# Kernel optimization log

Hardware: AMD Instinct MI355X
Metric: run time of the kernel (lower is better)

## Reference

```python
import jax, jax.numpy as jnp
import numpy as np

B, T, NMELS = 512, 180, 40
HID, NLAYER, PROJ = 768, 3, 256


def _lstm_layer(x, w_ih, w_hh, b):
    """PyTorch-convention LSTM layer. x: [B, T, D] -> h_seq: [B, T, H].
    Gate order i, f, g, o. b = b_ih + b_hh."""
    Bn = x.shape[0]
    H = w_hh.shape[1]
    # Input contribution for all timesteps at once: [T, B, 4H]
    xg = jnp.einsum('btd,gd->tbg', x, w_ih) + b

    def step(carry, xg_t):
        h, c = carry
        g = xg_t + h @ w_hh.T  # [B, 4H]
        i, f, gg, o = jnp.split(g, 4, axis=-1)
        i = jax.nn.sigmoid(i)
        f = jax.nn.sigmoid(f)
        gg = jnp.tanh(gg)
        o = jax.nn.sigmoid(o)
        c = f * c + i * gg
        h = o * jnp.tanh(c)
        return (h, c), h

    h0 = jnp.zeros((Bn, H), x.dtype)
    c0 = jnp.zeros((Bn, H), x.dtype)
    (_, _), hs = jax.lax.scan(step, (h0, c0), xg)  # hs: [T, B, H]
    return jnp.transpose(hs, (1, 0, 2))


def setup_inputs() -> dict:
    key = jax.random.key(0)
    ks = jax.random.split(key, 16)
    G = 4 * HID

    def xavier(k, shape):
        fan_out, fan_in = shape
        std = np.sqrt(2.0 / (fan_in + fan_out)).astype(np.float32)
        return jax.random.normal(k, shape, jnp.float32) * std

    inp = {
        'x': jax.random.normal(ks[0], (B, T, NMELS), jnp.float32),
        'w_ih0': xavier(ks[1], (G, NMELS)),
        'w_hh0': xavier(ks[2], (G, HID)),
        'b_ih0': jnp.zeros((G,), jnp.float32),
        'b_hh0': jnp.zeros((G,), jnp.float32),
        'w_ih1': xavier(ks[3], (G, HID)),
        'w_hh1': xavier(ks[4], (G, HID)),
        'b_ih1': jnp.zeros((G,), jnp.float32),
        'b_hh1': jnp.zeros((G,), jnp.float32),
        'w_ih2': xavier(ks[5], (G, HID)),
        'w_hh2': xavier(ks[6], (G, HID)),
        'b_ih2': jnp.zeros((G,), jnp.float32),
        'b_hh2': jnp.zeros((G,), jnp.float32),
        'proj_w': xavier(ks[7], (PROJ, HID)),
        'proj_b': jnp.zeros((PROJ,), jnp.float32),
    }
    return inp


def reference(x, w_ih0, w_hh0, b_ih0, b_hh0,
              w_ih1, w_hh1, b_ih1, b_hh1,
              w_ih2, w_hh2, b_ih2, b_hh2,
              proj_w, proj_b):
    h = _lstm_layer(x, w_ih0, w_hh0, b_ih0 + b_hh0)
    h = _lstm_layer(h, w_ih1, w_hh1, b_ih1 + b_hh1)
    h = _lstm_layer(h, w_ih2, w_hh2, b_ih2 + b_hh2)
    last = h[:, -1]                       # [B, HID] last timestep
    e = last @ proj_w.T + proj_b          # [B, PROJ]
    e = e / jnp.linalg.norm(e, axis=1, keepdims=True)
    return e
```

## Files before the change

kernel.cpp:

```cpp
#include <hip/hip_runtime.h>
#include <cstdint>
#include <cstddef>

using u16 = unsigned short;
using u32 = unsigned int;

typedef __attribute__((ext_vector_type(8)))  __bf16 bf16x8;
typedef __attribute__((ext_vector_type(16))) float  f32x16;

constexpr int kB   = 512;
constexpr int kT   = 180;
constexpr int kH   = 768;
constexpr int NBLK = 192;

constexpr int L0N  = 16 * 192 * 832;
constexpr int L12N = 16 * 192 * 1536;

constexpr int RING_SLOT_E = 24 * 512 * 32;
constexpr size_t RING_SZ  = (size_t)2 * RING_SLOT_E * 2;

constexpr size_t OFF_R0  = 256;
constexpr size_t OFF_R1  = OFF_R0 + RING_SZ;
constexpr size_t OFF_R2  = OFF_R1 + RING_SZ;
constexpr size_t OFF_PB  = OFF_R2 + RING_SZ;
constexpr size_t OFF_XT  = OFF_PB + (size_t)3 * 3072 * 4;
constexpr size_t OFF_W0  = OFF_XT + (size_t)kT * kB * 64 * 2;
constexpr size_t OFF_W1  = OFF_W0 + (size_t)L0N * 2;
constexpr size_t OFF_W2  = OFF_W1 + (size_t)L12N * 2;
constexpr size_t WS_NEED = OFF_W2 + (size_t)L12N * 2;

#define CLB __asm__ volatile("" ::: "memory")

__device__ __forceinline__ float bf2f(u16 u) {
  union { u32 i; float f; } v; v.i = ((u32)u) << 16; return v.f;
}
__device__ __forceinline__ u16 f2bf(float f) {
  union { float f; u32 i; } v; v.f = f;
  u32 r = v.i + 0x7fffu + ((v.i >> 16) & 1u);
  return (u16)(r >> 16);
}

typedef __attribute__((address_space(1))) const u32 as1_u32;
typedef __attribute__((address_space(3))) u32 as3_u32;
__device__ __forceinline__ void gload_lds16(const u16* g, u16* l) {
  __builtin_amdgcn_global_load_lds((as1_u32*)g, (as3_u32*)l, 16, 0, 0);
}

__global__ void k_zero(uint4* p, int n) {
  uint4 z = make_uint4(0u, 0u, 0u, 0u);
  for (int i = blockIdx.x * 256 + threadIdx.x; i < n; i += gridDim.x * 256) p[i] = z;
}

__global__ void k_pack_w(const float* __restrict__ wih0, const float* __restrict__ whh0,
                         const float* __restrict__ wih1, const float* __restrict__ whh1,
                         const float* __restrict__ wih2, const float* __restrict__ whh2,
                         u16* __restrict__ W0, u16* __restrict__ W1, u16* __restrict__ W2) {
  int idx = blockIdx.x * 256 + threadIdx.x;
  if (idx < L0N) {
    int col = idx / 832, k = idx - col * 832;
    int ntile = col / 192, p = col - ntile * 192;
    int g = p / 48, hc = p - g * 48;
    int gcol = g * 768 + ntile * 48 + hc;
    float v = (k < 40) ? wih0[gcol * 40 + k]
                       : ((k < 64) ? 0.f : whh0[(size_t)gcol * 768 + (k - 64)]);
    W0[idx] = f2bf(v);
  } else if (idx < L0N + L12N) {
    int li = idx - L0N;
    int col = li / 1536, k = li - col * 1536;
    int ntile = col / 192, p = col - ntile * 192;
    int g = p / 48, hc = p - g * 48;
    int gcol = g * 768 + ntile * 48 + hc;
    float v = (k < 768) ? wih1[(size_t)gcol * 768 + k] : whh1[(size_t)gcol * 768 + (k - 768)];
    W1[li] = f2bf(v);
  } else {
    int li = idx - (L0N + L12N);
    if (li < L12N) {
      int col = li / 1536, k = li - col * 1536;
      int ntile = col / 192, p = col - ntile * 192;
      int g = p / 48, hc = p - g * 48;
      int gcol = g * 768 + ntile * 48 + hc;
      float v = (k < 768) ? wih2[(size_t)gcol * 768 + k] : whh2[(size_t)gcol * 768 + (k - 768)];
      W2[li] = f2bf(v);
    }
  }
}

__global__ void k_pack_b(const float* __restrict__ bi0, const float* __restrict__ bh0,
                         const float* __restrict__ bi1, const float* __restrict__ bh1,
                         const float* __restrict__ bi2, const float* __restrict__ bh2,
                         float* __restrict__ pbo) {
  int idx = blockIdx.x * 256 + threadIdx.x;
  int l = idx / 3072, r = idx - l * 3072;
  int ntile = r / 192, p = r - ntile * 192;
  int g = p / 48, hc = p - g * 48;
  int gcol = g * 768 + ntile * 48 + hc;
  const float* bi = (l == 0) ? bi0 : ((l == 1) ? bi1 : bi2);
  const float* bh = (l == 0) ? bh0 : ((l == 1) ? bh1 : bh2);
  pbo[idx] = bi[gcol] + bh[gcol];
}

__global__ void k_xT(const float* __restrict__ x, u16* __restrict__ xT) {
  int idx = blockIdx.x * 256 + threadIdx.x;
  int t = idx / (512 * 64);
  int r = idx - t * 512 * 64;
  int b = r >> 6, j = r & 63;
  float v = (j < 40) ? x[((size_t)b * 180 + t) * 40 + j] : 0.f;
  xT[(size_t)t * 32768 + (size_t)(j >> 5) * 16384 + b * 32 + (j & 31)] = f2bf(v);
}

__global__ __launch_bounds__(256, 2) void k_lstm(
    const u16* __restrict__ xT,
    u16* __restrict__ ring0, u16* __restrict__ ring1, u16* __restrict__ ring2,
    const u16* __restrict__ W0, const u16* __restrict__ W1, const u16* __restrict__ W2,
    const float* __restrict__ pb, u32* __restrict__ bar) {
  __shared__ __align__(16) unsigned char smem[61440 + 768];
  u16*   scr = (u16*)smem;
  float* pbs = (float*)(smem + 61440);

  const int tid = threadIdx.x;
  const int bid = blockIdx.x;
  const int xcd = bid & 7, j0 = bid >> 3;
  const int g_    = (j0 >> 2) * 8 + xcd;
  const int mt    = j0 & 3;
  const int layer = g_ >> 4;
  const int ntile = g_ & 15;
  const int mrow0 = mt * 128;

  const u16* Wl     = (layer == 0) ? W0 : ((layer == 1) ? W1 : W2);
  const int  Kl     = (layer == 0) ? 832 : 1536;
  const int  KcIn   = (layer == 0) ? 2 : 24;
  const int  nch    = (layer == 0) ? 26 : 48;
  const u16* inseq  = (layer == 1) ? ring0 : ring1;
  u16*       ringS  = (layer == 0) ? ring0 : ((layer == 1) ? ring1 : ring2);
  const u16* bbase0 = Wl + (size_t)(ntile * 192) * Kl;

  for (int i = tid; i < 192; i += 256) pbs[i] = pb[layer * 3072 + ntile * 192 + i];

  const int wid = tid >> 6, lane = tid & 63;
  const int wm = wid & 1, wn = wid >> 1;
  const int l31 = lane & 31, lhi = lane >> 5;

  float c_reg[24];
#pragma unroll
  for (int i = 0; i < 24; i++) c_reg[i] = 0.f;

  for (int s = 0; s < kT + 2; ++s) {
    const int t = s - layer;
    if (t >= 0 && t < kT) {
      f32x16 acc[2][3];
#pragma unroll
      for (int mi = 0; mi < 2; mi++)
#pragma unroll
        for (int ni = 0; ni < 3; ni++)
#pragma unroll
          for (int r = 0; r < 16; r++) acc[mi][ni][r] = 0.f;

      const u16* inbase  = (layer == 0) ? (xT + (size_t)t * 32768)
                                        : (inseq + (size_t)(t & 1) * RING_SLOT_E);
      const u16* recbase = ringS + (size_t)((t - 1) & 1) * RING_SLOT_E;

      auto stage = [&](int c, int st) {
        u16* sbA = (u16*)(smem + st * 20480);
        u16* sbB = sbA + 4096;
        const u16* abase = (c < KcIn) ? (inbase + (size_t)c * 16384)
                                      : (recbase + (size_t)(c - KcIn) * 16384);
#pragma unroll
        for (int k = 0; k < 2; k++) {
          const int e = tid + k * 256;
          const int row = e >> 2, sp = e & 3;
          const int so = sp ^ ((row >> 1) & 3);
          gload_lds16(abase + (size_t)(mrow0 + row) * 32 + so * 8, sbA + (size_t)e * 8);
        }
        const u16* bb = bbase0 + c * 32;
#pragma unroll
        for (int k = 0; k < 3; k++) {
          const int e = tid + k * 256;
          const int col = e >> 2, sp = e & 3;
          const int so = sp ^ ((col >> 1) & 3);
          gload_lds16(bb + (size_t)col * Kl + so * 8, sbB + (size_t)e * 8);
        }
      };

      stage(0, 0);
      stage(1, 1);
      for (int c = 0; c < nch; ++c) {
        CLB;
        if (c == nch - 1) __builtin_amdgcn_s_waitcnt(0xF70);
        else              __builtin_amdgcn_s_waitcnt(0xF75);
        __builtin_amdgcn_s_barrier();
        CLB;
        if (c + 2 < nch) stage(c + 2, (c + 2) % 3);
        const u16* sA = (const u16*)(smem + (c % 3) * 20480);
        const u16* sB = sA + 4096;
        const int wsw = (l31 >> 1) & 3;
#pragma unroll
        for (int kk = 0; kk < 2; kk++) {
          const int sl = (((kk << 1) | lhi) ^ wsw) << 3;
          bf16x8 a0 = *(const bf16x8*)(sA + (wm * 64 +      l31) * 32 + sl);
          bf16x8 a1 = *(const bf16x8*)(sA + (wm * 64 + 32 + l31) * 32 + sl);
          const int c0 = wn * 96 + l31;
          bf16x8 b0 = *(const bf16x8*)(sB + (c0     ) * 32 + sl);
          bf16x8 b1 = *(const bf16x8*)(sB + (c0 + 32) * 32 + sl);
          bf16x8 b2 = *(const bf16x8*)(sB + (c0 + 64) * 32 + sl);
          acc[0][0] = __builtin_amdgcn_mfma_f32_32x32x16_bf16(a0, b0, acc[0][0], 0, 0, 0);
          acc[0][1] = __builtin_amdgcn_mfma_f32_32x32x16_bf16(a0, b1, acc[0][1], 0, 0, 0);
          acc[0][2] = __builtin_amdgcn_mfma_f32_32x32x16_bf16(a0, b2, acc[0][2], 0, 0, 0);
          acc[1][0] = __builtin_amdgcn_mfma_f32_32x32x16_bf16(a1, b0, acc[1][0], 0, 0, 0);
          acc[1][1] = __builtin_amdgcn_mfma_f32_32x32x16_bf16(a1, b1, acc[1][1], 0, 0, 0);
          acc[1][2] = __builtin_amdgcn_mfma_f32_32x32x16_bf16(a1, b2, acc[1][2], 0, 0, 0);
        }
      }
      __syncthreads();
#pragma unroll
      for (int mi = 0; mi < 2; mi++) {
#pragma unroll
        for (int ni = 0; ni < 3; ni++) {
          const int pcol = wn * 96 + ni * 32 + l31;
          const int gg = pcol / 48;
          const float bias = pbs[pcol];
#pragma unroll
          for (int r = 0; r < 16; r++) {
            const int rowl = wm * 64 + mi * 32 + (r & 3) + ((r >> 2) << 3) + (lhi << 2);
            float v = acc[mi][ni][r] + bias;
            v = (gg == 2) ? tanhf(v) : (1.f / (1.f + __expf(-v)));
            scr[rowl * 192 + pcol] = f2bf(v);
          }
        }
      }
      __syncthreads();
      u16* hout = ringS + (size_t)(t & 1) * RING_SLOT_E;
#pragma unroll
      for (int jj = 0; jj < 24; jj++) {
        const int idx = jj * 256 + tid;
        const int row = idx / 48;
        const int hc  = idx - row * 48;
        const float iv = bf2f(scr[row * 192       + hc]);
        const float fv = bf2f(scr[row * 192 +  48 + hc]);
        const float gv = bf2f(scr[row * 192 +  96 + hc]);
        const float ov = bf2f(scr[row * 192 + 144 + hc]);
        const float cn = fv * c_reg[jj] + iv * gv;
        c_reg[jj] = cn;
        const int colg = ntile * 48 + hc;
        hout[(size_t)(colg >> 5) * 16384 + (size_t)(mrow0 + row) * 32 + (colg & 31)]
            = f2bf(ov * tanhf(cn));
      }
    }
    __syncthreads();
    if (tid == 0) {
      __hip_atomic_fetch_add(bar, 1u, __ATOMIC_RELEASE, __HIP_MEMORY_SCOPE_AGENT);
      const u32 goal = (u32)(s + 1) * (u32)NBLK;
      u32 tries = 0;
      while (__hip_atomic_load(bar, __ATOMIC_RELAXED, __HIP_MEMORY_SCOPE_AGENT) < goal) {
        __builtin_amdgcn_s_sleep(8);
        if (++tries > 100000u) break;
      }
      __threadfence();
    }
    __syncthreads();
  }
}

__global__ __launch_bounds__(256) void k_proj(const u16* __restrict__ hlast,
                                              const float* __restrict__ pw,
                                              const float* __restrict__ pbv,
                                              float* __restrict__ out) {
  __shared__ float hs[8 * 768];
  __shared__ float wred[4 * 8];
  __shared__ float inv[8];
  const int tid = threadIdx.x;
  const int r0 = blockIdx.x * 8;
  for (int i = tid; i < 8 * 768; i += 256) {
    const int b = i / 768, col = i - b * 768;
    hs[i] = bf2f(hlast[(size_t)(col >> 5) * 16384 + (size_t)(r0 + b) * 32 + (col & 31)]);
  }
  __syncthreads();
  float acc[8];
#pragma unroll
  for (int r = 0; r < 8; r++) acc[r] = 0.f;
  const float* wrow = pw + (size_t)tid * 768;
  for (int k = 0; k < 768; k++) {
    float w = wrow[k];
#pragma unroll
    for (int r = 0; r < 8; r++) acc[r] += hs[r * 768 + k] * w;
  }
  const float bv = pbv[tid];
#pragma unroll
  for (int r = 0; r < 8; r++) acc[r] += bv;
  const int lane = tid & 63, w4 = tid >> 6;
#pragma unroll
  for (int r = 0; r < 8; r++) {
    float v = acc[r] * acc[r];
#pragma unroll
    for (int off = 32; off > 0; off >>= 1) v += __shfl_xor(v, off);
    if (lane == 0) wred[w4 * 8 + r] = v;
  }
  __syncthreads();
  if (tid < 8) {
    float sum = wred[tid] + wred[8 + tid] + wred[16 + tid] + wred[24 + tid];
    inv[tid] = 1.f / sqrtf(sum);
  }
  __syncthreads();
#pragma unroll
  for (int r = 0; r < 8; r++) out[(size_t)(r0 + r) * 256 + tid] = acc[r] * inv[r];
}

extern "C" void kernel_launch(void* const* d_in, const int* in_sizes, int n_in,
                              void* d_out, int out_size, void* d_ws, size_t ws_size,
                              hipStream_t stream) {
  const float* x    = (const float*)d_in[0];
  const float* wih0 = (const float*)d_in[1];
  const float* whh0 = (const float*)d_in[2];
  const float* bi0  = (const float*)d_in[3];
  const float* bh0  = (const float*)d_in[4];
  const float* wih1 = (const float*)d_in[5];
  const float* whh1 = (const float*)d_in[6];
  const float* bi1  = (const float*)d_in[7];
  const float* bh1  = (const float*)d_in[8];
  const float* wih2 = (const float*)d_in[9];
  const float* whh2 = (const float*)d_in[10];
  const float* bi2  = (const float*)d_in[11];
  const float* bh2  = (const float*)d_in[12];
  const float* pw   = (const float*)d_in[13];
  const float* pbv  = (const float*)d_in[14];

  if (ws_size < WS_NEED) return;

  char* ws  = (char*)d_ws;
  u32*  bar = (u32*)(ws + 0);
  u16*  r0  = (u16*)(ws + OFF_R0);
  u16*  r1  = (u16*)(ws + OFF_R1);
  u16*  r2  = (u16*)(ws + OFF_R2);
  float* pb = (float*)(ws + OFF_PB);
  u16*  xT  = (u16*)(ws + OFF_XT);
  u16*  W0  = (u16*)(ws + OFF_W0);
  u16*  W1  = (u16*)(ws + OFF_W1);
  u16*  W2  = (u16*)(ws + OFF_W2);

  hipLaunchKernelGGL(k_zero, dim3(512), dim3(256), 0, stream,
                     (uint4*)ws, (int)(OFF_PB / 16));
  hipLaunchKernelGGL(k_pack_w, dim3((L0N + 2 * L12N + 255) / 256), dim3(256), 0, stream,
                     wih0, whh0, wih1, whh1, wih2, whh2, W0, W1, W2);
  hipLaunchKernelGGL(k_pack_b, dim3(36), dim3(256), 0, stream,
                     bi0, bh0, bi1, bh1, bi2, bh2, pb);
  hipLaunchKernelGGL(k_xT, dim3(kT * kB * 64 / 256), dim3(256), 0, stream, x, xT);

  {
    const u16* xTc = xT; const float* pbc = pb;
    const u16 *W0c = W0, *W1c = W1, *W2c = W2;
    u16 *r0m = r0, *r1m = r1, *r2m = r2; u32* barm = bar;
    void* kargs[] = {(void*)&xTc, (void*)&r0m, (void*)&r1m, (void*)&r2m,
                     (void*)&W0c, (void*)&W1c, (void*)&W2c, (void*)&pbc, (void*)&barm};
    hipLaunchCooperativeKernel((void*)k_lstm, dim3(NBLK), dim3(256), kargs, 0, stream);
  }

  hipLaunchKernelGGL(k_proj, dim3(64), dim3(256), 0, stream,
                     r2 + (size_t)((kT - 1) & 1) * RING_SLOT_E, pw, pbv, (float*)d_out);
}
```

Before: 9.799 ms.

## Deepen LSTM LDS pipeline to six stages with dynamic shared memory

Adds a k_lstm_deep variant that uses about 120 KB of dynamic LDS for six prefetch stages instead of three. It keeps five chunks in flight, with vmcnt waits tuned to the remaining chunk count, and runs at one block per CU. Activation and recurrent loads now carry a cache-policy bit, and the __threadfence after the grid barrier spin is removed. The aim is to hide global-load latency in the per-timestep GEMM. The cost is lower occupancy and a reliance on the cache bits, rather than the fence, to make cross-block data visible.

```diff
diff --git a/kernel.cpp b/kernel.cpp
--- a/kernel.cpp
+++ b/kernel.cpp
@@ -29,6 +29,10 @@
 constexpr size_t OFF_W2  = OFF_W1 + (size_t)L12N * 2;
 constexpr size_t WS_NEED = OFF_W2 + (size_t)L12N * 2;
 
+constexpr int    NSTAGE   = 6;
+constexpr size_t STAGE_SZ = 20480;
+constexpr size_t DYN_LDS  = NSTAGE * STAGE_SZ + 768;
+
 #define CLB __asm__ volatile("" ::: "memory")
 
 __device__ __forceinline__ float bf2f(u16 u) {
@@ -44,6 +48,9 @@
 typedef __attribute__((address_space(3))) u32 as3_u32;
 __device__ __forceinline__ void gload_lds16(const u16* g, u16* l) {
   __builtin_amdgcn_global_load_lds((as1_u32*)g, (as3_u32*)l, 16, 0, 0);
+}
+__device__ __forceinline__ void gload_lds16_dc(const u16* g, u16* l) {
+  __builtin_amdgcn_global_load_lds((as1_u32*)g, (as3_u32*)l, 16, 0, 16);
 }
 
 __global__ void k_zero(uint4* p, int n) {
@@ -108,156 +115,171 @@
   xT[(size_t)t * 32768 + (size_t)(j >> 5) * 16384 + b * 32 + (j & 31)] = f2bf(v);
 }
 
+#define LSTM_BODY(SMEM_DECL, SMEM_PTR, NSTG, DEEP)                                     \
+  SMEM_DECL;                                                                           \
+  u16*   scr = (u16*)(SMEM_PTR);                                                       \
+  float* pbs = (float*)((SMEM_PTR) + (size_t)(NSTG) * STAGE_SZ);                       \
+  const int tid = threadIdx.x;                                                         \
+  const int bid = blockIdx.x;                                                          \
+  const int xcd = bid & 7, j0 = bid >> 3;                                              \
+  const int g_    = (j0 >> 2) * 8 + xcd;                                               \
+  const int mt    = j0 & 3;                                                            \
+  const int layer = g_ >> 4;                                                           \
+  const int ntile = g_ & 15;                                                           \
+  const int mrow0 = mt * 128;                                                          \
+  const u16* Wl     = (layer == 0) ? W0 : ((layer == 1) ? W1 : W2);                    \
+  const int  Kl     = (layer == 0) ? 832 : 1536;                                       \
+  const int  KcIn   = (layer == 0) ? 2 : 24;                                           \
+  const int  nch    = (layer == 0) ? 26 : 48;                                          \
+  const u16* inseq  = (layer == 1) ? ring0 : ring1;                                    \
+  u16*       ringS  = (layer == 0) ? ring0 : ((layer == 1) ? ring1 : ring2);           \
+  const u16* bbase0 = Wl + (size_t)(ntile * 192) * Kl;                                 \
+  for (int i = tid; i < 192; i += 256) pbs[i] = pb[layer * 3072 + ntile * 192 + i];    \
+  const int wid = tid >> 6, lane = tid & 63;                                           \
+  const int wm = wid & 1, wn = wid >> 1;                                               \
+  const int l31 = lane & 31, lhi = lane >> 5;                                          \
+  float c_reg[24];                                                                     \
+  _Pragma("unroll")                                                                    \
+  for (int i = 0; i < 24; i++) c_reg[i] = 0.f;                                         \
+  for (int s = 0; s < kT + 2; ++s) {                                                   \
+    const int t = s - layer;                                                           \
+    if (t >= 0 && t < kT) {                                                            \
+      f32x16 acc[2][3];                                                                \
+      _Pragma("unroll")                                                                \
+      for (int mi = 0; mi < 2; mi++)                                                   \
+        for (int ni = 0; ni < 3; ni++)                                                 \
+          for (int r = 0; r < 16; r++) acc[mi][ni][r] = 0.f;                           \
+      const u16* inbase  = (layer == 0) ? (xT + (size_t)t * 32768)                     \
+                                        : (inseq + (size_t)(t & 1) * RING_SLOT_E);     \
+      const u16* recbase = ringS + (size_t)((t - 1) & 1) * RING_SLOT_E;                \
+      auto stage = [&](int c, int st) {                                                \
+        u16* sbA = (u16*)((SMEM_PTR) + (size_t)st * STAGE_SZ);                         \
+        u16* sbB = sbA + 4096;                                                         \
+        const bool rsrc = (layer != 0) || (c >= KcIn);                                 \
+        const u16* abase = (c < KcIn) ? (inbase + (size_t)c * 16384)                   \
+                                      : (recbase + (size_t)(c - KcIn) * 16384);        \
+        _Pragma("unroll")                                                              \
+        for (int k = 0; k < 2; k++) {                                                  \
+          const int e = tid + k * 256;                                                 \
+          const int row = e >> 2, sp = e & 3;                                          \
+          const int so = sp ^ ((row >> 1) & 3);                                        \
+          const u16* ga = abase + (size_t)(mrow0 + row) * 32 + so * 8;                 \
+          u16*       la = sbA + (size_t)e * 8;                                         \
+          if (rsrc) gload_lds16_dc(ga, la);                                            \
+          else      gload_lds16(ga, la);                                               \
+        }                                                                              \
+        const u16* bb = bbase0 + c * 32;                                               \
+        _Pragma("unroll")                                                              \
+        for (int k = 0; k < 3; k++) {                                                  \
+          const int e = tid + k * 256;                                                 \
+          const int col = e >> 2, sp = e & 3;                                          \
+          const int so = sp ^ ((col >> 1) & 3);                                        \
+          gload_lds16(bb + (size_t)col * Kl + so * 8, sbB + (size_t)e * 8);            \
+        }                                                                              \
+      };                                                                               \
+      if (DEEP) { stage(0,0); stage(1,1); stage(2,2); stage(3,3); stage(4,4); }        \
+      else      { stage(0,0); stage(1,1); }                                            \
+      for (int c = 0; c < nch; ++c) {                                                  \
+        CLB;                                                                           \
+        const int rem = nch - 1 - c;                                                   \
+        if (DEEP) {                                                                    \
+          switch (rem > 4 ? 4 : rem) {                                                 \
+            case 0:  __builtin_amdgcn_s_waitcnt(0x0F70); break;         \
+            case 1:  __builtin_amdgcn_s_waitcnt(0x0F75); break;         \
+            case 2:  __builtin_amdgcn_s_waitcnt(0x0F7A); break;         \
+            case 3:  __builtin_amdgcn_s_waitcnt(0x0F7F); break;         \
+            default: __builtin_amdgcn_s_waitcnt(0x4F74); break;         \
+          }                                                                            \
+        } else {                                                                       \
+          if (rem == 0) __builtin_amdgcn_s_waitcnt(0x0F70);             \
+          else          __builtin_amdgcn_s_waitcnt(0x0F75);             \
+        }                                                                              \
+        __builtin_amdgcn_s_barrier();                                                  \
+        CLB;                                                                           \
+        const int pf = DEEP ? 5 : 2;                                                   \
+        if (c + pf < nch) stage(c + pf, (c + pf) % (NSTG));                            \
+        const u16* sA = (const u16*)((SMEM_PTR) + (size_t)(c % (NSTG)) * STAGE_SZ);    \
+        const u16* sB = sA + 4096;                                                     \
+        const int wsw = (l31 >> 1) & 3;                                                \
+        _Pragma("unroll")                                                              \
+        for (int kk = 0; kk < 2; kk++) {                                               \
+          const int sl = (((kk << 1) | lhi) ^ wsw) << 3;                               \
+          bf16x8 a0 = *(const bf16x8*)(sA + (wm * 64 +      l31) * 32 + sl);           \
+          bf16x8 a1 = *(const bf16x8*)(sA + (wm * 64 + 32 + l31) * 32 + sl);           \
+          const int c0 = wn * 96 + l31;                                                \
+          bf16x8 b0 = *(const bf16x8*)(sB + (c0     ) * 32 + sl);                      \
+          bf16x8 b1 = *(const bf16x8*)(sB + (c0 + 32) * 32 + sl);                      \
+          bf16x8 b2 = *(const bf16x8*)(sB + (c0 + 64) * 32 + sl);                      \
+          acc[0][0] = __builtin_amdgcn_mfma_f32_32x32x16_bf16(a0, b0, acc[0][0],0,0,0);\
+          acc[0][1] = __builtin_amdgcn_mfma_f32_32x32x16_bf16(a0, b1, acc[0][1],0,0,0);\
+          acc[0][2] = __builtin_amdgcn_mfma_f32_32x32x16_bf16(a0, b2, acc[0][2],0,0,0);\
+          acc[1][0] = __builtin_amdgcn_mfma_f32_32x32x16_bf16(a1, b0, acc[1][0],0,0,0);\
+          acc[1][1] = __builtin_amdgcn_mfma_f32_32x32x16_bf16(a1, b1, acc[1][1],0,0,0);\
+          acc[1][2] = __builtin_amdgcn_mfma_f32_32x32x16_bf16(a1, b2, acc[1][2],0,0,0);\
+        }                                                                              \
+      }                                                                                \
+      __syncthreads();                                                                 \
+      _Pragma("unroll")                                                                \
+      for (int mi = 0; mi < 2; mi++) {                                                 \
+        _Pragma("unroll")                                                              \
+        for (int ni = 0; ni < 3; ni++) {                                               \
+          const int pcol = wn * 96 + ni * 32 + l31;                                    \
+          const int gg = pcol / 48;                                                    \
+          const float bias = pbs[pcol];                                                \
+          _Pragma("unroll")                                                            \
+          for (int r = 0; r < 16; r++) {                                               \
+            const int rowl = wm * 64 + mi * 32 + (r & 3) + ((r >> 2) << 3) + (lhi << 2);\
+            float v = acc[mi][ni][r] + bias;                                           \
+            v = (gg == 2) ? tanhf(v) : (1.f / (1.f + __expf(-v)));                     \
+            scr[rowl * 192 + pcol] = f2bf(v);                                          \
+          }                                                                            \
+        }                                                                              \
+      }                                                                                \
+      __syncthreads();                                                                 \
+      u16* hout = ringS + (size_t)(t & 1) * RING_SLOT_E;                               \
+      _Pragma("unroll")                                                                \
+      for (int jj = 0; jj < 24; jj++) {                                                \
+        const int idx = jj * 256 + tid;                                                \
+        const int row = idx / 48;                                                      \
+        const int hc  = idx - row * 48;                                                \
+        const float iv = bf2f(scr[row * 192       + hc]);                              \
+        const float fv = bf2f(scr[row * 192 +  48 + hc]);                              \
+        const float gv = bf2f(scr[row * 192 +  96 + hc]);                              \
+        const float ov = bf2f(scr[row * 192 + 144 + hc]);                              \
+        const float cn = fv * c_reg[jj] + iv * gv;                                     \
+        c_reg[jj] = cn;                                                                \
+        const int colg = ntile * 48 + hc;                                              \
+        hout[(size_t)(colg >> 5) * 16384 + (size_t)(mrow0 + row) * 32 + (colg & 31)]   \
+            = f2bf(ov * tanhf(cn));                                                    \
+      }                                                                                \
+    }                                                                                  \
+    __syncthreads();                                                                   \
+    if (tid == 0) {                                                                    \
+      __hip_atomic_fetch_add(bar, 1u, __ATOMIC_RELEASE, __HIP_MEMORY_SCOPE_AGENT);     \
+      const u32 goal = (u32)(s + 1) * (u32)NBLK;                                       \
+      u32 tries = 0;                                                                   \
+      while (__hip_atomic_load(bar, __ATOMIC_RELAXED, __HIP_MEMORY_SCOPE_AGENT) < goal) {\
+        __builtin_amdgcn_s_sleep(8);                                                   \
+        if (++tries > 100000u) break;                                                  \
+      }                                                                                \
+    }                                                                                  \
+    __syncthreads();                                                                   \
+  }
+
+__global__ __launch_bounds__(256, 1) void k_lstm_deep(
+    const u16* __restrict__ xT,
+    u16* __restrict__ ring0, u16* __restrict__ ring1, u16* __restrict__ ring2,
+    const u16* __restrict__ W0, const u16* __restrict__ W1, const u16* __restrict__ W2,
+    const float* __restrict__ pb, u32* __restrict__ bar) {
+  LSTM_BODY(extern __shared__ __align__(16) unsigned char smem[], smem, NSTAGE, 1)
+}
+
 __global__ __launch_bounds__(256, 2) void k_lstm(
     const u16* __restrict__ xT,
     u16* __restrict__ ring0, u16* __restrict__ ring1, u16* __restrict__ ring2,
     const u16* __restrict__ W0, const u16* __restrict__ W1, const u16* __restrict__ W2,
     const float* __restrict__ pb, u32* __restrict__ bar) {
-  __shared__ __align__(16) unsigned char smem[61440 + 768];
-  u16*   scr = (u16*)smem;
-  float* pbs = (float*)(smem + 61440);
-
-  const int tid = threadIdx.x;
-  const int bid = blockIdx.x;
-  const int xcd = bid & 7, j0 = bid >> 3;
-  const int g_    = (j0 >> 2) * 8 + xcd;
-  const int mt    = j0 & 3;
-  const int layer = g_ >> 4;
-  const int ntile = g_ & 15;
-  const int mrow0 = mt * 128;
-
-  const u16* Wl     = (layer == 0) ? W0 : ((layer == 1) ? W1 : W2);
-  const int  Kl     = (layer == 0) ? 832 : 1536;
-  const int  KcIn   = (layer == 0) ? 2 : 24;
-  const int  nch    = (layer == 0) ? 26 : 48;
-  const u16* inseq  = (layer == 1) ? ring0 : ring1;
-  u16*       ringS  = (layer == 0) ? ring0 : ((layer == 1) ? ring1 : ring2);
-  const u16* bbase0 = Wl + (size_t)(ntile * 192) * Kl;
-
-  for (int i = tid; i < 192; i += 256) pbs[i] = pb[layer * 3072 + ntile * 192 + i];
-
-  const int wid = tid >> 6, lane = tid & 63;
-  const int wm = wid & 1, wn = wid >> 1;
-  const int l31 = lane & 31, lhi = lane >> 5;
-
-  float c_reg[24];
-#pragma unroll
-  for (int i = 0; i < 24; i++) c_reg[i] = 0.f;
-
-  for (int s = 0; s < kT + 2; ++s) {
-    const int t = s - layer;
-    if (t >= 0 && t < kT) {
-      f32x16 acc[2][3];
-#pragma unroll
-      for (int mi = 0; mi < 2; mi++)
-#pragma unroll
-        for (int ni = 0; ni < 3; ni++)
-#pragma unroll
-          for (int r = 0; r < 16; r++) acc[mi][ni][r] = 0.f;
-
-      const u16* inbase  = (layer == 0) ? (xT + (size_t)t * 32768)
-                                        : (inseq + (size_t)(t & 1) * RING_SLOT_E);
-      const u16* recbase = ringS + (size_t)((t - 1) & 1) * RING_SLOT_E;
-
-      auto stage = [&](int c, int st) {
-        u16* sbA = (u16*)(smem + st * 20480);
-        u16* sbB = sbA + 4096;
-        const u16* abase = (c < KcIn) ? (inbase + (size_t)c * 16384)
-                                      : (recbase + (size_t)(c - KcIn) * 16384);
-#pragma unroll
-        for (int k = 0; k < 2; k++) {
-          const int e = tid + k * 256;
-          const int row = e >> 2, sp = e & 3;
-          const int so = sp ^ ((row >> 1) & 3);
-          gload_lds16(abase + (size_t)(mrow0 + row) * 32 + so * 8, sbA + (size_t)e * 8);
-        }
-        const u16* bb = bbase0 + c * 32;
-#pragma unroll
-        for (int k = 0; k < 3; k++) {
-          const int e = tid + k * 256;
-          const int col = e >> 2, sp = e & 3;
-          const int so = sp ^ ((col >> 1) & 3);
-          gload_lds16(bb + (size_t)col * Kl + so * 8, sbB + (size_t)e * 8);
-        }
-      };
-
-      stage(0, 0);
-      stage(1, 1);
-      for (int c = 0; c < nch; ++c) {
-        CLB;
-        if (c == nch - 1) __builtin_amdgcn_s_waitcnt(0xF70);
-        else              __builtin_amdgcn_s_waitcnt(0xF75);
-        __builtin_amdgcn_s_barrier();
-        CLB;
-        if (c + 2 < nch) stage(c + 2, (c + 2) % 3);
-        const u16* sA = (const u16*)(smem + (c % 3) * 20480);
-        const u16* sB = sA + 4096;
-        const int wsw = (l31 >> 1) & 3;
-#pragma unroll
-        for (int kk = 0; kk < 2; kk++) {
-          const int sl = (((kk << 1) | lhi) ^ wsw) << 3;
-          bf16x8 a0 = *(const bf16x8*)(sA + (wm * 64 +      l31) * 32 + sl);
-          bf16x8 a1 = *(const bf16x8*)(sA + (wm * 64 + 32 + l31) * 32 + sl);
-          const int c0 = wn * 96 + l31;
-          bf16x8 b0 = *(const bf16x8*)(sB + (c0     ) * 32 + sl);
-          bf16x8 b1 = *(const bf16x8*)(sB + (c0 + 32) * 32 + sl);
-          bf16x8 b2 = *(const bf16x8*)(sB + (c0 + 64) * 32 + sl);
-          acc[0][0] = __builtin_amdgcn_mfma_f32_32x32x16_bf16(a0, b0, acc[0][0], 0, 0, 0);
-          acc[0][1] = __builtin_amdgcn_mfma_f32_32x32x16_bf16(a0, b1, acc[0][1], 0, 0, 0);
-          acc[0][2] = __builtin_amdgcn_mfma_f32_32x32x16_bf16(a0, b2, acc[0][2], 0, 0, 0);
-          acc[1][0] = __builtin_amdgcn_mfma_f32_32x32x16_bf16(a1, b0, acc[1][0], 0, 0, 0);
-          acc[1][1] = __builtin_amdgcn_mfma_f32_32x32x16_bf16(a1, b1, acc[1][1], 0, 0, 0);
-          acc[1][2] = __builtin_amdgcn_mfma_f32_32x32x16_bf16(a1, b2, acc[1][2], 0, 0, 0);
-        }
-      }
-      __syncthreads();
-#pragma unroll
-      for (int mi = 0; mi < 2; mi++) {
-#pragma unroll
-        for (int ni = 0; ni < 3; ni++) {
-          const int pcol = wn * 96 + ni * 32 + l31;
-          const int gg = pcol / 48;
-          const float bias = pbs[pcol];
-#pragma unroll
-          for (int r = 0; r < 16; r++) {
-            const int rowl = wm * 64 + mi * 32 + (r & 3) + ((r >> 2) << 3) + (lhi << 2);
-            float v = acc[mi][ni][r] + bias;
-            v = (gg == 2) ? tanhf(v) : (1.f / (1.f + __expf(-v)));
-            scr[rowl * 192 + pcol] = f2bf(v);
-          }
-        }
-      }
-      __syncthreads();
-      u16* hout = ringS + (size_t)(t & 1) * RING_SLOT_E;
-#pragma unroll
-      for (int jj = 0; jj < 24; jj++) {
-        const int idx = jj * 256 + tid;
-        const int row = idx / 48;
-        const int hc  = idx - row * 48;
-        const float iv = bf2f(scr[row * 192       + hc]);
-        const float fv = bf2f(scr[row * 192 +  48 + hc]);
-        const float gv = bf2f(scr[row * 192 +  96 + hc]);
-        const float ov = bf2f(scr[row * 192 + 144 + hc]);
-        const float cn = fv * c_reg[jj] + iv * gv;
-        c_reg[jj] = cn;
-        const int colg = ntile * 48 + hc;
-        hout[(size_t)(colg >> 5) * 16384 + (size_t)(mrow0 + row) * 32 + (colg & 31)]
-            = f2bf(ov * tanhf(cn));
-      }
-    }
-    __syncthreads();
-    if (tid == 0) {
-      __hip_atomic_fetch_add(bar, 1u, __ATOMIC_RELEASE, __HIP_MEMORY_SCOPE_AGENT);
-      const u32 goal = (u32)(s + 1) * (u32)NBLK;
-      u32 tries = 0;
-      while (__hip_atomic_load(bar, __ATOMIC_RELAXED, __HIP_MEMORY_SCOPE_AGENT) < goal) {
-        __builtin_amdgcn_s_sleep(8);
-        if (++tries > 100000u) break;
-      }
-      __threadfence();
-    }
-    __syncthreads();
-  }
+  LSTM_BODY(__shared__ __align__(16) unsigned char smem[61440 + 768], smem, 3, 0)
 }
 
 __global__ __launch_bounds__(256) void k_proj(const u16* __restrict__ hlast,
@@ -325,6 +347,17 @@
 
   if (ws_size < WS_NEED) return;
 
+  static int use_deep = -1;
+  if (use_deep < 0) {
+    hipError_t e1 = hipFuncSetAttribute((const void*)k_lstm_deep,
+                                        hipFuncAttributeMaxDynamicSharedMemorySize,
+                                        (int)DYN_LDS);
+    int nb = 0;
+    hipError_t e2 = hipOccupancyMaxActiveBlocksPerMultiprocessor(
+        &nb, k_lstm_deep, 256, (size_t)DYN_LDS);
+    use_deep = (e1 == hipSuccess && e2 == hipSuccess && nb >= 1) ? 1 : 0;
+  }
+
   char* ws  = (char*)d_ws;
   u32*  bar = (u32*)(ws + 0);
   u16*  r0  = (u16*)(ws + OFF_R0);
@@ -350,7 +383,12 @@
     u16 *r0m = r0, *r1m = r1, *r2m = r2; u32* barm = bar;
     void* kargs[] = {(void*)&xTc, (void*)&r0m, (void*)&r1m, (void*)&r2m,
                      (void*)&W0c, (void*)&W1c, (void*)&W2c, (void*)&pbc, (void*)&barm};
-    hipLaunchCooperativeKernel((void*)k_lstm, dim3(NBLK), dim3(256), kargs, 0, stream);
+    if (use_deep) {
+      hipLaunchCooperativeKernel((void*)k_lstm_deep, dim3(NBLK), dim3(256), kargs,
+                                 (unsigned int)DYN_LDS, stream);
+    } else {
+      hipLaunchCooperativeKernel((void*)k_lstm, dim3(NBLK), dim3(256), kargs, 0, stream);
+    }
   }
 
   hipLaunchKernelGGL(k_proj, dim3(64), dim3(256), 0, stream,
```

New measurement: 9.411 ms. -4.0%, faster.

## Replace global grid barrier with per-tile dataflow flags and split into 384 blocks

Applied to the files above, without the earlier changes.

Swaps the grid-wide barrier after every wavefront step for per-(layer, row-tile) counters: each block waits only for its input layer's tile, its own layer's previous step, and the next layer's progress, which lets the three layers pipeline loosely. A new 384-block variant halves the M tile to 64 rows with three blocks per CU, for more parallelism and less work per block on each step. The old 192-block kernel is kept as a fallback, chosen at runtime from an occupancy query. This adds more flag polling traffic and smaller MFMA tiles that reuse the B operand less.

```diff
diff --git a/kernel.cpp b/kernel.cpp
--- a/kernel.cpp
+++ b/kernel.cpp
@@ -11,7 +11,8 @@
 constexpr int kB   = 512;
 constexpr int kT   = 180;
 constexpr int kH   = 768;
-constexpr int NBLK = 192;
+constexpr int NBLK3 = 384;
+constexpr int NBLK2 = 192;
 
 constexpr int L0N  = 16 * 192 * 832;
 constexpr int L12N = 16 * 192 * 1536;
@@ -19,7 +20,7 @@
 constexpr int RING_SLOT_E = 24 * 512 * 32;
 constexpr size_t RING_SZ  = (size_t)2 * RING_SLOT_E * 2;
 
-constexpr size_t OFF_R0  = 256;
+constexpr size_t OFF_R0  = 16384;
 constexpr size_t OFF_R1  = OFF_R0 + RING_SZ;
 constexpr size_t OFF_R2  = OFF_R1 + RING_SZ;
 constexpr size_t OFF_PB  = OFF_R2 + RING_SZ;
@@ -108,11 +109,162 @@
   xT[(size_t)t * 32768 + (size_t)(j >> 5) * 16384 + b * 32 + (j & 31)] = f2bf(v);
 }
 
-__global__ __launch_bounds__(256, 2) void k_lstm(
+__global__ __launch_bounds__(256, 3) void k_lstm384(
     const u16* __restrict__ xT,
     u16* __restrict__ ring0, u16* __restrict__ ring1, u16* __restrict__ ring2,
     const u16* __restrict__ W0, const u16* __restrict__ W1, const u16* __restrict__ W2,
-    const float* __restrict__ pb, u32* __restrict__ bar) {
+    const float* __restrict__ pb, u32* __restrict__ flg) {
+  __shared__ __align__(16) unsigned char smem[49152];
+  u16* scr = (u16*)smem;
+
+  const int tid = threadIdx.x;
+  const int bid = blockIdx.x;
+  const int xcd = bid & 7, j0 = bid >> 3;
+  const int g_    = (j0 >> 3) * 8 + xcd;
+  const int mt    = j0 & 7;
+  const int layer = g_ >> 4;
+  const int ntile = g_ & 15;
+  const int mrow0 = mt * 64;
+
+  const u16* Wl     = (layer == 0) ? W0 : ((layer == 1) ? W1 : W2);
+  const int  Kl     = (layer == 0) ? 832 : 1536;
+  const int  KcIn   = (layer == 0) ? 2 : 24;
+  const int  nch    = (layer == 0) ? 26 : 48;
+  const u16* inseq  = (layer == 1) ? ring0 : ring1;
+  u16*       ringS  = (layer == 0) ? ring0 : ((layer == 1) ? ring1 : ring2);
+  const u16* bbase0 = Wl + (size_t)(ntile * 192) * Kl;
+
+  u32* Fself = flg + (size_t)(((layer << 3) | mt) * 64);
+  u32* Fin   = flg + (size_t)((((layer - 1) << 3) | mt) * 64);
+  u32* Fnxt  = flg + (size_t)((((layer + 1) << 3) | mt) * 64);
+
+  const int wid = tid >> 6, lane = tid & 63;
+  const int wm = wid & 1, wn = wid >> 1;
+  const int l31 = lane & 31, lhi = lane >> 5;
+
+  float bias_r[3];
+#pragma unroll
+  for (int ni = 0; ni < 3; ni++)
+    bias_r[ni] = pb[layer * 3072 + ntile * 192 + wn * 96 + ni * 32 + l31];
+
+  float c_reg[12];
+#pragma unroll
+  for (int i = 0; i < 12; i++) c_reg[i] = 0.f;
+
+  for (int t = 0; t < kT; ++t) {
+    if (tid == 0) {
+      auto spinf = [&](u32* f, u32 goal) {
+        u32 tries = 0;
+        while (__hip_atomic_load(f, __ATOMIC_RELAXED, __HIP_MEMORY_SCOPE_AGENT) < goal) {
+          __builtin_amdgcn_s_sleep(4);
+          if (++tries > 400000u) break;
+        }
+      };
+      if (layer >= 1)           spinf(Fin,   16u * (u32)(t + 1));
+      if (t >= 1)               spinf(Fself, 16u * (u32)t);
+      if (layer <= 1 && t >= 2) spinf(Fnxt,  16u * (u32)(t - 1));
+      __threadfence();
+    }
+    __syncthreads();
+
+    f32x16 acc[3];
+#pragma unroll
+    for (int ni = 0; ni < 3; ni++)
+#pragma unroll
+      for (int r = 0; r < 16; r++) acc[ni][r] = 0.f;
+
+    const u16* inbase  = (layer == 0) ? (xT + (size_t)t * 32768)
+                                      : (inseq + (size_t)(t & 1) * RING_SLOT_E);
+    const u16* recbase = ringS + (size_t)((t - 1) & 1) * RING_SLOT_E;
+
+    auto stage = [&](int c, int st) {
+      u16* sbA = (u16*)(smem + (size_t)st * 16384);
+      u16* sbB = sbA + 2048;
+      const u16* abase = (c < KcIn) ? (inbase + (size_t)c * 16384)
+                                    : (recbase + (size_t)(c - KcIn) * 16384);
+      {
+        const int e = tid;
+        const int row = e >> 2, sp = e & 3;
+        const int so = sp ^ ((row >> 1) & 3);
+        gload_lds16(abase + (size_t)(mrow0 + row) * 32 + so * 8, sbA + (size_t)e * 8);
+      }
+      const u16* bb = bbase0 + c * 32;
+#pragma unroll
+      for (int k = 0; k < 3; k++) {
+        const int e = tid + k * 256;
+        const int col = e >> 2, sp = e & 3;
+        const int so = sp ^ ((col >> 1) & 3);
+        gload_lds16(bb + (size_t)col * Kl + so * 8, sbB + (size_t)e * 8);
+      }
+    };
+
+    stage(0, 0);
+    stage(1, 1);
+    for (int c = 0; c < nch; ++c) {
+      CLB;
+      if (c == nch - 1) __builtin_amdgcn_s_waitcnt(0x0F70);
+      else              __builtin_amdgcn_s_waitcnt(0x0F74);
+      __builtin_amdgcn_s_barrier();
+      CLB;
+      if (c + 2 < nch) stage(c + 2, (c + 2) % 3);
+      const u16* sA = (const u16*)(smem + (size_t)(c % 3) * 16384);
+      const u16* sB = sA + 2048;
+      const int wsw = (l31 >> 1) & 3;
+#pragma unroll
+      for (int kk = 0; kk < 2; kk++) {
+        const int sl = (((kk << 1) | lhi) ^ wsw) << 3;
+        bf16x8 a0 = *(const bf16x8*)(sA + (wm * 32 + l31) * 32 + sl);
+        const int c0 = wn * 96 + l31;
+        bf16x8 b0 = *(const bf16x8*)(sB + (c0     ) * 32 + sl);
+        bf16x8 b1 = *(const bf16x8*)(sB + (c0 + 32) * 32 + sl);
+        bf16x8 b2 = *(const bf16x8*)(sB + (c0 + 64) * 32 + sl);
+        acc[0] = __builtin_amdgcn_mfma_f32_32x32x16_bf16(a0, b0, acc[0], 0, 0, 0);
+        acc[1] = __builtin_amdgcn_mfma_f32_32x32x16_bf16(a0, b1, acc[1], 0, 0, 0);
+        acc[2] = __builtin_amdgcn_mfma_f32_32x32x16_bf16(a0, b2, acc[2], 0, 0, 0);
+      }
+    }
+    __syncthreads();
+#pragma unroll
+    for (int ni = 0; ni < 3; ni++) {
+      const int pcol = wn * 96 + ni * 32 + l31;
+      const int gate = pcol / 48;
+      const float bias = bias_r[ni];
+#pragma unroll
+      for (int r = 0; r < 16; r++) {
+        const int rowl = wm * 32 + (r & 3) + ((r >> 2) << 3) + (lhi << 2);
+        float v = acc[ni][r] + bias;
+        v = (gate == 2) ? tanhf(v) : (1.f / (1.f + __expf(-v)));
+        scr[rowl * 192 + pcol] = f2bf(v);
+      }
+    }
+    __syncthreads();
+    u16* hout = ringS + (size_t)(t & 1) * RING_SLOT_E;
+#pragma unroll
+    for (int jj = 0; jj < 12; jj++) {
+      const int idx = jj * 256 + tid;
+      const int row = idx / 48;
+      const int hc  = idx - row * 48;
+      const float iv = bf2f(scr[row * 192       + hc]);
+      const float fv = bf2f(scr[row * 192 +  48 + hc]);
+      const float gv = bf2f(scr[row * 192 +  96 + hc]);
+      const float ov = bf2f(scr[row * 192 + 144 + hc]);
+      const float cn = fv * c_reg[jj] + iv * gv;
+      c_reg[jj] = cn;
+      const int colg = ntile * 48 + hc;
+      hout[(size_t)(colg >> 5) * 16384 + (size_t)(mrow0 + row) * 32 + (colg & 31)]
+          = f2bf(ov * tanhf(cn));
+    }
+    __syncthreads();
+    if (tid == 0)
+      __hip_atomic_fetch_add(Fself, 1u, __ATOMIC_RELEASE, __HIP_MEMORY_SCOPE_AGENT);
+  }
+}
+
+__global__ __launch_bounds__(256, 2) void k_lstm192(
+    const u16* __restrict__ xT,
+    u16* __restrict__ ring0, u16* __restrict__ ring1, u16* __restrict__ ring2,
+    const u16* __restrict__ W0, const u16* __restrict__ W1, const u16* __restrict__ W2,
+    const float* __restrict__ pb, u32* __restrict__ flg) {
   __shared__ __align__(16) unsigned char smem[61440 + 768];
   u16*   scr = (u16*)smem;
   float* pbs = (float*)(smem + 61440);
@@ -134,6 +286,10 @@
   u16*       ringS  = (layer == 0) ? ring0 : ((layer == 1) ? ring1 : ring2);
   const u16* bbase0 = Wl + (size_t)(ntile * 192) * Kl;
 
+  u32* Fself = flg + (size_t)(((layer << 3) | (mt << 1)) * 64);
+  u32* Fin   = flg + (size_t)((((layer - 1) << 3) | (mt << 1)) * 64);
+  u32* Fnxt  = flg + (size_t)((((layer + 1) << 3) | (mt << 1)) * 64);
+
   for (int i = tid; i < 192; i += 256) pbs[i] = pb[layer * 3072 + ntile * 192 + i];
 
   const int wid = tid >> 6, lane = tid & 63;
@@ -144,119 +300,122 @@
 #pragma unroll
   for (int i = 0; i < 24; i++) c_reg[i] = 0.f;
 
-  for (int s = 0; s < kT + 2; ++s) {
-    const int t = s - layer;
-    if (t >= 0 && t < kT) {
-      f32x16 acc[2][3];
-#pragma unroll
-      for (int mi = 0; mi < 2; mi++)
-#pragma unroll
-        for (int ni = 0; ni < 3; ni++)
-#pragma unroll
-          for (int r = 0; r < 16; r++) acc[mi][ni][r] = 0.f;
-
-      const u16* inbase  = (layer == 0) ? (xT + (size_t)t * 32768)
-                                        : (inseq + (size_t)(t & 1) * RING_SLOT_E);
-      const u16* recbase = ringS + (size_t)((t - 1) & 1) * RING_SLOT_E;
-
-      auto stage = [&](int c, int st) {
-        u16* sbA = (u16*)(smem + st * 20480);
-        u16* sbB = sbA + 4096;
-        const u16* abase = (c < KcIn) ? (inbase + (size_t)c * 16384)
-                                      : (recbase + (size_t)(c - KcIn) * 16384);
-#pragma unroll
-        for (int k = 0; k < 2; k++) {
-          const int e = tid + k * 256;
-          const int row = e >> 2, sp = e & 3;
-          const int so = sp ^ ((row >> 1) & 3);
-          gload_lds16(abase + (size_t)(mrow0 + row) * 32 + so * 8, sbA + (size_t)e * 8);
-        }
-        const u16* bb = bbase0 + c * 32;
-#pragma unroll
-        for (int k = 0; k < 3; k++) {
-          const int e = tid + k * 256;
-          const int col = e >> 2, sp = e & 3;
-          const int so = sp ^ ((col >> 1) & 3);
-          gload_lds16(bb + (size_t)col * Kl + so * 8, sbB + (size_t)e * 8);
+  for (int t = 0; t < kT; ++t) {
+    if (tid == 0) {
+      auto spinf = [&](u32* f, u32 goal) {
+        u32 tries = 0;
+        while (__hip_atomic_load(f, __ATOMIC_RELAXED, __HIP_MEMORY_SCOPE_AGENT) < goal) {
+          __builtin_amdgcn_s_sleep(4);
+          if (++tries > 400000u) break;
         }
       };
-
-      stage(0, 0);
-      stage(1, 1);
-      for (int c = 0; c < nch; ++c) {
-        CLB;
-        if (c == nch - 1) __builtin_amdgcn_s_waitcnt(0xF70);
-        else              __builtin_amdgcn_s_waitcnt(0xF75);
-        __builtin_amdgcn_s_barrier();
-        CLB;
-        if (c + 2 < nch) stage(c + 2, (c + 2) % 3);
-        const u16* sA = (const u16*)(smem + (c % 3) * 20480);
-        const u16* sB = sA + 4096;
-        const int wsw = (l31 >> 1) & 3;
-#pragma unroll
-        for (int kk = 0; kk < 2; kk++) {
-          const int sl = (((kk << 1) | lhi) ^ wsw) << 3;
-          bf16x8 a0 = *(const bf16x8*)(sA + (wm * 64 +      l31) * 32 + sl);
-          bf16x8 a1 = *(const bf16x8*)(sA + (wm * 64 + 32 + l31) * 32 + sl);
-          const int c0 = wn * 96 + l31;
-          bf16x8 b0 = *(const bf16x8*)(sB + (c0     ) * 32 + sl);
-          bf16x8 b1 = *(const bf16x8*)(sB + (c0 + 32) * 32 + sl);
-          bf16x8 b2 = *(const bf16x8*)(sB + (c0 + 64) * 32 + sl);
-          acc[0][0] = __builtin_amdgcn_mfma_f32_32x32x16_bf16(a0, b0, acc[0][0], 0, 0, 0);
-          acc[0][1] = __builtin_amdgcn_mfma_f32_32x32x16_bf16(a0, b1, acc[0][1], 0, 0, 0);
-          acc[0][2] = __builtin_amdgcn_mfma_f32_32x32x16_bf16(a0, b2, acc[0][2], 0, 0, 0);
-          acc[1][0] = __builtin_amdgcn_mfma_f32_32x32x16_bf16(a1, b0, acc[1][0], 0, 0, 0);
-          acc[1][1] = __builtin_amdgcn_mfma_f32_32x32x16_bf16(a1, b1, acc[1][1], 0, 0, 0);
-          acc[1][2] = __builtin_amdgcn_mfma_f32_32x32x16_bf16(a1, b2, acc[1][2], 0, 0, 0);
+      if (layer >= 1)           spinf(Fin,   16u * (u32)(t + 1));
+      if (t >= 1)               spinf(Fself, 16u * (u32)t);
+      if (layer <= 1 && t >= 2) spinf(Fnxt,  16u * (u32)(t - 1));
+      __threadfence();
+    }
+    __syncthreads();
+
+    f32x16 acc[2][3];
+#pragma unroll
+    for (int mi = 0; mi < 2; mi++)
+#pragma unroll
+      for (int ni = 0; ni < 3; ni++)
+#pragma unroll
+        for (int r = 0; r < 16; r++) acc[mi][ni][r] = 0.f;
+
+    const u16* inbase  = (layer == 0) ? (xT + (size_t)t * 32768)
+                                      : (inseq + (size_t)(t & 1) * RING_SLOT_E);
+    const u16* recbase = ringS + (size_t)((t - 1) & 1) * RING_SLOT_E;
+
+    auto stage = [&](int c, int st) {
+      u16* sbA = (u16*)(smem + st * 20480);
+      u16* sbB = sbA + 4096;
+      const u16* abase = (c < KcIn) ? (inbase + (size_t)c * 16384)
+                                    : (recbase + (size_t)(c - KcIn) * 16384);
+#pragma unroll
+      for (int k = 0; k < 2; k++) {
+        const int e = tid + k * 256;
+        const int row = e >> 2, sp = e & 3;
+        const int so = sp ^ ((row >> 1) & 3);
+        gload_lds16(abase + (size_t)(mrow0 + row) * 32 + so * 8, sbA + (size_t)e * 8);
+      }
+      const u16* bb = bbase0 + c * 32;
+#pragma unroll
+      for (int k = 0; k < 3; k++) {
+        const int e = tid + k * 256;
+        const int col = e >> 2, sp = e & 3;
+        const int so = sp ^ ((col >> 1) & 3);
+        gload_lds16(bb + (size_t)col * Kl + so * 8, sbB + (size_t)e * 8);
+      }
+    };
+
+    stage(0, 0);
+    stage(1, 1);
+    for (int c = 0; c < nch; ++c) {
+      CLB;
+      if (c == nch - 1) __builtin_amdgcn_s_waitcnt(0x0F70);
+      else              __builtin_amdgcn_s_waitcnt(0x0F75);
+      __builtin_amdgcn_s_barrier();
+      CLB;
+      if (c + 2 < nch) stage(c + 2, (c + 2) % 3);
+      const u16* sA = (const u16*)(smem + (c % 3) * 20480);
+      const u16* sB = sA + 4096;
+      const int wsw = (l31 >> 1) & 3;
+#pragma unroll
+      for (int kk = 0; kk < 2; kk++) {
+        const int sl = (((kk << 1) | lhi) ^ wsw) << 3;
+        bf16x8 a0 = *(const bf16x8*)(sA + (wm * 64 +      l31) * 32 + sl);
+        bf16x8 a1 = *(const bf16x8*)(sA + (wm * 64 + 32 + l31) * 32 + sl);
+        const int c0 = wn * 96 + l31;
+        bf16x8 b0 = *(const bf16x8*)(sB + (c0     ) * 32 + sl);
+        bf16x8 b1 = *(const bf16x8*)(sB + (c0 + 32) * 32 + sl);
+        bf16x8 b2 = *(const bf16x8*)(sB + (c0 + 64) * 32 + sl);
+        acc[0][0] = __builtin_amdgcn_mfma_f32_32x32x16_bf16(a0, b0, acc[0][0], 0, 0, 0);
+        acc[0][1] = __builtin_amdgcn_mfma_f32_32x32x16_bf16(a0, b1, acc[0][1], 0, 0, 0);
+        acc[0][2] = __builtin_amdgcn_mfma_f32_32x32x16_bf16(a0, b2, acc[0][2], 0, 0, 0);
+        acc[1][0] = __builtin_amdgcn_mfma_f32_32x32x16_bf16(a1, b0, acc[1][0], 0, 0, 0);
+        acc[1][1] = __builtin_amdgcn_mfma_f32_32x32x16_bf16(a1, b1, acc[1][1], 0, 0, 0);
+        acc[1][2] = __builtin_amdgcn_mfma_f32_32x32x16_bf16(a1, b2, acc[1][2], 0, 0, 0);
+      }
+    }
+    __syncthreads();
+#pragma unroll
+    for (int mi = 0; mi < 2; mi++) {
+#pragma unroll
+      for (int ni = 0; ni < 3; ni++) {
+        const int pcol = wn * 96 + ni * 32 + l31;
+        const int gg = pcol / 48;
+        const float bias = pbs[pcol];
+#pragma unroll
+        for (int r = 0; r < 16; r++) {
+          const int rowl = wm * 64 + mi * 32 + (r & 3) + ((r >> 2) << 3) + (lhi << 2);
+          float v = acc[mi][ni][r] + bias;
+          v = (gg == 2) ? tanhf(v) : (1.f / (1.f + __expf(-v)));
+          scr[rowl * 192 + pcol] = f2bf(v);
         }
       }
-      __syncthreads();
-#pragma unroll
-      for (int mi = 0; mi < 2; mi++) {
-#pragma unroll
-        for (int ni = 0; ni < 3; ni++) {
-          const int pcol = wn * 96 + ni * 32 + l31;
-          const int gg = pcol / 48;
-          const float bias = pbs[pcol];
-#pragma unroll
-          for (int r = 0; r < 16; r++) {
-            const int rowl = wm * 64 + mi * 32 + (r & 3) + ((r >> 2) << 3) + (lhi << 2);
-            float v = acc[mi][ni][r] + bias;
-            v = (gg == 2) ? tanhf(v) : (1.f / (1.f + __expf(-v)));
-            scr[rowl * 192 + pcol] = f2bf(v);
-          }
-        }
-      }
-      __syncthreads();
-      u16* hout = ringS + (size_t)(t & 1) * RING_SLOT_E;
-#pragma unroll
-      for (int jj = 0; jj < 24; jj++) {
-        const int idx = jj * 256 + tid;
-        const int row = idx / 48;
-        const int hc  = idx - row * 48;
-        const float iv = bf2f(scr[row * 192       + hc]);
-        const float fv = bf2f(scr[row * 192 +  48 + hc]);
-        const float gv = bf2f(scr[row * 192 +  96 + hc]);
-        const float ov = bf2f(scr[row * 192 + 144 + hc]);
-        const float cn = fv * c_reg[jj] + iv * gv;
-        c_reg[jj] = cn;
-        const int colg = ntile * 48 + hc;
-        hout[(size_t)(colg >> 5) * 16384 + (size_t)(mrow0 + row) * 32 + (colg & 31)]
-            = f2bf(ov * tanhf(cn));
-      }
-    }
-    __syncthreads();
-    if (tid == 0) {
-      __hip_atomic_fetch_add(bar, 1u, __ATOMIC_RELEASE, __HIP_MEMORY_SCOPE_AGENT);
-      const u32 goal = (u32)(s + 1) * (u32)NBLK;
-      u32 tries = 0;
-      while (__hip_atomic_load(bar, __ATOMIC_RELAXED, __HIP_MEMORY_SCOPE_AGENT) < goal) {
-        __builtin_amdgcn_s_sleep(8);
-        if (++tries > 100000u) break;
-      }
-      __threadfence();
-    }
-    __syncthreads();
+    }
+    __syncthreads();
+    u16* hout = ringS + (size_t)(t & 1) * RING_SLOT_E;
+#pragma unroll
+    for (int jj = 0; jj < 24; jj++) {
+      const int idx = jj * 256 + tid;
+      const int row = idx / 48;
+      const int hc  = idx - row * 48;
+      const float iv = bf2f(scr[row * 192       + hc]);
+      const float fv = bf2f(scr[row * 192 +  48 + hc]);
+      const float gv = bf2f(scr[row * 192 +  96 + hc]);
+      const float ov = bf2f(scr[row * 192 + 144 + hc]);
+      const float cn = fv * c_reg[jj] + iv * gv;
+      c_reg[jj] = cn;
+      const int colg = ntile * 48 + hc;
+      hout[(size_t)(colg >> 5) * 16384 + (size_t)(mrow0 + row) * 32 + (colg & 31)]
+          = f2bf(ov * tanhf(cn));
+    }
+    __syncthreads();
+    if (tid == 0)
+      __hip_atomic_fetch_add(Fself, 1u, __ATOMIC_RELEASE, __HIP_MEMORY_SCOPE_AGENT);
   }
 }
 
@@ -325,8 +484,19 @@
 
   if (ws_size < WS_NEED) return;
 
+  static int mode = -1;
+  if (mode < 0) {
+    int nb = 0;
+    hipError_t e1 = hipOccupancyMaxActiveBlocksPerMultiprocessor(&nb, k_lstm384, 256, 0);
+    int dev = 0; hipGetDevice(&dev);
+    hipDeviceProp_t props{};
+    hipError_t e2 = hipGetDeviceProperties(&props, dev);
+    mode = (e1 == hipSuccess && e2 == hipSuccess &&
+            nb * props.multiProcessorCount >= NBLK3) ? 1 : 0;
+  }
+
   char* ws  = (char*)d_ws;
-  u32*  bar = (u32*)(ws + 0);
+  u32*  flg = (u32*)(ws + 0);
   u16*  r0  = (u16*)(ws + OFF_R0);
   u16*  r1  = (u16*)(ws + OFF_R1);
   u16*  r2  = (u16*)(ws + OFF_R2);
@@ -347,10 +517,18 @@
   {
     const u16* xTc = xT; const float* pbc = pb;
     const u16 *W0c = W0, *W1c = W1, *W2c = W2;
-    u16 *r0m = r0, *r1m = r1, *r2m = r2; u32* barm = bar;
+    u16 *r0m = r0, *r1m = r1, *r2m = r2; u32* flgm = flg;
     void* kargs[] = {(void*)&xTc, (void*)&r0m, (void*)&r1m, (void*)&r2m,
-                     (void*)&W0c, (void*)&W1c, (void*)&W2c, (void*)&pbc, (void*)&barm};
-    hipLaunchCooperativeKernel((void*)k_lstm, dim3(NBLK), dim3(256), kargs, 0, stream);
+                     (void*)&W0c, (void*)&W1c, (void*)&W2c, (void*)&pbc, (void*)&flgm};
+    if (mode == 1) {
+      hipError_t le = hipLaunchCooperativeKernel((void*)k_lstm384, dim3(NBLK3),
+                                                 dim3(256), kargs, 0, stream);
+      if (le != hipSuccess) mode = 0;
+    }
+    if (mode == 0) {
+      hipLaunchCooperativeKernel((void*)k_lstm192, dim3(NBLK2), dim3(256),
+                                 kargs, 0, stream);
+    }
   }
 
   hipLaunchKernelGGL(k_proj, dim3(64), dim3(256), 0, stream,
```

After: 8.986 ms. -8.3%, faster.
